# Kernel optimization log

Hardware: AMD Instinct MI355X
Metric: run time of the kernel (lower is better)

The kernel has to match this reference:

```python
import jax, jax.numpy as jnp
import numpy as np

B, S, D, H = 2, 2048, 1024, 16
HD = D // H  # head dim = 64


def setup_inputs() -> dict:
    key = jax.random.key(0)
    ks = jax.random.split(key, 9)
    s_in = 1.0 / np.sqrt(D)
    s_out = 1.0 / np.sqrt(HD)
    return {
        "x": jax.random.normal(ks[0], (B, S, D), jnp.float32),
        "Wq": jax.random.normal(ks[1], (D, H, HD), jnp.float32) * s_in,
        "bq": jnp.zeros((H, HD), jnp.float32),
        "Wk": jax.random.normal(ks[2], (D, H, HD), jnp.float32) * s_in,
        "bk": jnp.zeros((H, HD), jnp.float32),
        "Wv": jax.random.normal(ks[3], (D, H, HD), jnp.float32) * s_in,
        "bv": jnp.zeros((H, HD), jnp.float32),
        "Wo": jax.random.normal(ks[4], (H, HD, D), jnp.float32) * s_out,
        "bo": jnp.zeros((D,), jnp.float32),
    }


def reference(x, Wq, bq, Wk, bk, Wv, bv, Wo, bo):
    # QKV projections: [B,S,D] -> [B,S,H,HD]
    q = jnp.einsum("bsd,dhk->bshk", x, Wq) + bq
    k = jnp.einsum("bsd,dhk->bshk", x, Wk) + bk
    v = jnp.einsum("bsd,dhk->bshk", x, Wv) + bv

    # scaled dot-product attention (matches nnx.dot_product_attention)
    scale = jnp.asarray(1.0 / np.sqrt(HD), q.dtype)
    scores = jnp.einsum("bqhk,bshk->bhqs", q * scale, k)  # [B,H,S,S]
    attn = jax.nn.softmax(scores, axis=-1)
    y = jnp.einsum("bhqs,bshk->bqhk", attn, v)  # [B,S,H,HD]

    # exclusive post-processing: subtract projection onto L2-normalized v
    eps = jnp.asarray(1e-12, v.dtype)
    v_norm = v * jax.lax.rsqrt(jnp.sum(jnp.square(v), axis=-1, keepdims=True) + eps)
    y = y - jnp.sum(y * v_norm, axis=-1, keepdims=True) * v_norm

    # output projection: [B,S,H,HD] -> [B,S,D]
    out = jnp.einsum("bshk,hkd->bsd", y, Wo) + bo
    return out  # dropout is identity (deterministic=True)
```

## Files before the change

kernel.cpp:

```cpp
#include <hip/hip_runtime.h>

#define BB 2
#define SS 2048
#define DD 1024
#define HH 16
#define HDD 64

typedef __attribute__((ext_vector_type(4))) float f32x4;
typedef __attribute__((ext_vector_type(8))) short short8;
typedef __attribute__((ext_vector_type(4))) short short4v;

__device__ __forceinline__ short f2bf(float f) {
    union { float f; unsigned u; } a; a.f = f;
    unsigned r = a.u + 0x7fffu + ((a.u >> 16) & 1u);
    return (short)(r >> 16);
}
__device__ __forceinline__ float bf2f(short s) {
    union { unsigned u; float f; } a; a.u = ((unsigned)(unsigned short)s) << 16;
    return a.f;
}
__device__ __forceinline__ float fast_exp2(float x) {
    float r;
    asm("v_exp_f32 %0, %1\n\ts_nop 0" : "=v"(r) : "v"(x));
    return r;
}
__device__ __forceinline__ unsigned cvt_pk_bf16(float lo, float hi) {
    unsigned r;
    asm("v_cvt_pk_bf16_f32 %0, %1, %2" : "=v"(r) : "v"(lo), "v"(hi));
    return r;
}

#define GLD16(gp, lp) __builtin_amdgcn_global_load_lds( \
    (const __attribute__((address_space(1))) void*)(gp), \
    (__attribute__((address_space(3))) void*)(lp), 16, 0, 0)

__global__ __launch_bounds__(256) void conv_all(
    const float* __restrict__ x,
    const float* __restrict__ Wq, const float* __restrict__ Wk,
    const float* __restrict__ Wv, const float* __restrict__ Wo,
    short* __restrict__ xb, short* __restrict__ Wt, short* __restrict__ Wot,
    float qscale)
{
    const int z = blockIdx.z;
    if (z == 4) {
        const int id = blockIdx.x * 16 + blockIdx.y;
        const size_t base = (size_t)id * 16384 + threadIdx.x * 8;
        #pragma unroll
        for (int it = 0; it < 8; ++it) {
            const size_t i = base + (size_t)it * 2048;
            f32x4 a = *(const f32x4*)(x + i);
            f32x4 b = *(const f32x4*)(x + i + 4);
            short8 o;
            #pragma unroll
            for (int j = 0; j < 4; j++) { o[j] = f2bf(a[j]); o[j + 4] = f2bf(b[j]); }
            *(short8*)(xb + i) = o;
        }
        return;
    }
    __shared__ float t[64][65];
    const float* src = (z == 0) ? Wq : (z == 1) ? Wk : (z == 2) ? Wv : Wo;
    short* dst = (z < 3) ? (Wt + (size_t)z * 1048576) : Wot;
    const float scale = (z == 0) ? qscale : 1.f;

    const int tid = threadIdx.x;
    const int c = tid & 63, rg = tid >> 6;
    const int bi = blockIdx.x * 64, bj = blockIdx.y * 64;
    #pragma unroll
    for (int i = 0; i < 16; i++)
        t[rg * 16 + i][c] = src[(size_t)(bi + rg * 16 + i) * 1024 + bj + c];
    __syncthreads();
    #pragma unroll
    for (int i = 0; i < 16; i++)
        dst[(size_t)(bj + rg * 16 + i) * 1024 + bi + c] = f2bf(scale * t[c][rg * 16 + i]);
}

template<int KIND>
__global__ __launch_bounds__(256, 2) void gemm_mfma(
    const short* __restrict__ A, const short* __restrict__ Bt,
    const float* __restrict__ b0, const float* __restrict__ b1,
    const float* __restrict__ b2, float qscale,
    short* __restrict__ oQ, short* __restrict__ oK, short* __restrict__ oV,
    float* __restrict__ oF)
{
    constexpr int BM = (KIND == 0) ? 128 : 64;
    constexpr int FM = BM / 32;
    constexpr int ASH = BM * 64;
    constexpr int BUFSTR = ASH + 8192;

    __shared__ short lds[2 * BUFSTR];
    const int tid = threadIdx.x;
    const int lane = tid & 63;
    const int ln15 = lane & 15, g = lane >> 4;
    const int swl = ln15 & 7;
    const int wid = tid >> 6;
    const int wm = wid >> 1, wn = wid & 1;
    const int bm = blockIdx.x * BM;
    const int bn = blockIdx.y * 128;
    const bool vpath = (KIND == 0) && (blockIdx.y >= 16);

    f32x4 acc[FM][4];
    #pragma unroll
    for (int i = 0; i < FM; i++)
        #pragma unroll
        for (int j = 0; j < 4; j++) acc[i][j] = (f32x4){0.f, 0.f, 0.f, 0.f};

    const int sr = lane >> 3, cs = lane & 7;
    const int sc8 = (cs ^ sr) << 3;
    const short* Ak = A;
    const short* Bk = Bt;
    int aoff[FM], adst[FM], boff[4], bdst[4];
    #pragma unroll
    for (int j = 0; j < FM; j++) {
        aoff[j] = (bm + wid * (BM / 4) + j * 8 + sr) * 1024 + sc8;
        adst[j] = (wid * (BM / 4) + j * 8) * 64;
    }
    #pragma unroll
    for (int j = 0; j < 4; j++) {
        boff[j] = (bn + wid * 32 + j * 8 + sr) * 1024 + sc8;
        bdst[j] = ASH + (wid * 32 + j * 8) * 64;
    }

    auto stage = [&](int BUF) {
        #pragma unroll
        for (int j = 0; j < FM; j++)
            GLD16(Ak + aoff[j], &lds[BUF * BUFSTR + adst[j]]);
        #pragma unroll
        for (int j = 0; j < 4; j++)
            GLD16(Bk + boff[j], &lds[BUF * BUFSTR + bdst[j]]);
        Ak += 64; Bk += 64;
    };

    const char* ldsc = (const char*)lds;
    int aB[2], bB[2];
    #pragma unroll
    for (int kk = 0; kk < 2; kk++) {
        aB[kk] = (wm * (BM / 2) + ln15) * 128 + ((((kk << 2) | g) ^ swl) << 4);
        bB[kk] = ASH * 2 + (wn * 64 + ln15) * 128 + ((((kk << 2) | g) ^ swl) << 4);
    }

    auto tilec = [&](int BUF) {
        #pragma unroll
        for (int kk = 0; kk < 2; kk++) {
            short8 af[FM], bf[4];
            #pragma unroll
            for (int f = 0; f < FM; f++)
                af[f] = *(const short8*)(ldsc + BUF * (BUFSTR * 2) + aB[kk] + f * 2048);
            #pragma unroll
            for (int f = 0; f < 4; f++)
                bf[f] = *(const short8*)(ldsc + BUF * (BUFSTR * 2) + bB[kk] + f * 2048);
            if (!vpath) {
                #pragma unroll
                for (int fm = 0; fm < FM; fm++)
                    #pragma unroll
                    for (int fn = 0; fn < 4; fn++)
                        acc[fm][fn] = __builtin_amdgcn_mfma_f32_16x16x32_bf16(
                            bf[fn], af[fm], acc[fm][fn], 0, 0, 0);
            } else {
                #pragma unroll
                for (int fm = 0; fm < FM; fm++)
                    #pragma unroll
                    for (int fn = 0; fn < 4; fn++)
                        acc[fm][fn] = __builtin_amdgcn_mfma_f32_16x16x32_bf16(
                            af[fm], bf[fn], acc[fm][fn], 0, 0, 0);
            }
        }
    };

    stage(0);
    asm volatile("s_waitcnt vmcnt(0)" ::: "memory");
    __builtin_amdgcn_s_barrier();

    #pragma unroll 1
    for (int i = 0; i < 7; ++i) {
        stage(1);
        tilec(0);
        asm volatile("s_waitcnt vmcnt(0) lgkmcnt(0)" ::: "memory");
        __builtin_amdgcn_s_barrier();
        stage(0);
        tilec(1);
        asm volatile("s_waitcnt vmcnt(0) lgkmcnt(0)" ::: "memory");
        __builtin_amdgcn_s_barrier();
    }
    stage(1);
    tilec(0);
    asm volatile("s_waitcnt vmcnt(0) lgkmcnt(0)" ::: "memory");
    __builtin_amdgcn_s_barrier();
    tilec(1);

    const int n_base = bn + wn * 64;

    if constexpr (KIND == 1) {
        #pragma unroll
        for (int fn = 0; fn < 4; fn++) {
            const int n0 = n_base + fn * 16 + 4 * g;
            const f32x4 b4 = *(const f32x4*)(b0 + n0);
            #pragma unroll
            for (int fm = 0; fm < FM; fm++) {
                const int t = bm + wm * (BM / 2) + fm * 16 + ln15;
                f32x4 o = acc[fm][fn] + b4;
                *(f32x4*)(oF + (size_t)t * 1024 + n0) = o;
            }
        }
    } else if (!vpath) {
        const bool isq = (n_base < 1024);
        short* dst = isq ? oQ : oK;
        const float* bp = isq ? b0 : b1;
        const float scl = isq ? qscale : 1.f;
        #pragma unroll
        for (int fn = 0; fn < 4; fn++) {
            const int n0 = n_base + fn * 16 + 4 * g;
            const int nl = n0 & 1023;
            f32x4 b4 = *(const f32x4*)(bp + nl);
            b4 *= scl;
            const int h = nl >> 6, d = nl & 63;
            #pragma unroll
            for (int fm = 0; fm < FM; fm++) {
                const int t = bm + wm * (BM / 2) + fm * 16 + ln15;
                const int b = t >> 11, s = t & 2047;
                short4v pk = { f2bf(acc[fm][fn][0] + b4[0]), f2bf(acc[fm][fn][1] + b4[1]),
                               f2bf(acc[fm][fn][2] + b4[2]), f2bf(acc[fm][fn][3] + b4[3]) };
                *(short4v*)(dst + ((size_t)(b * HH + h) * SS + s) * HDD + d) = pk;
            }
        }
    } else {
        #pragma unroll
        for (int fn = 0; fn < 4; fn++) {
            const int nf = n_base + fn * 16 + ln15;
            const int nl = nf - 2048;
            const float bb = b2[nl];
            const int h = nl >> 6, d = nl & 63;
            #pragma unroll
            for (int fm = 0; fm < FM; fm++) {
                const int t0 = bm + wm * (BM / 2) + fm * 16 + 4 * g;
                const int b = t0 >> 11;
                const int sb = (t0 & 2047) & ~63;
                const int pos = g * 16 + (fm & 1) * 4 + ((fm >> 1) & 1) * 8;
                short4v pk = { f2bf(acc[fm][fn][0] + bb), f2bf(acc[fm][fn][1] + bb),
                               f2bf(acc[fm][fn][2] + bb), f2bf(acc[fm][fn][3] + bb) };
                *(short4v*)(oV + ((size_t)(b * HH + h) * HDD + d) * SS + sb + pos) = pk;
            }
        }
    }
}

__global__ __launch_bounds__(256, 2) void attn_mfma_kernel(
    const short* __restrict__ Qh, const short* __restrict__ Kh,
    const short* __restrict__ Vt, short* __restrict__ yb)
{
    __shared__ short lds[32768];

    const int lane = threadIdx.x & 63;
    const int wid  = threadIdx.x >> 6;
    const int ln15 = lane & 15;
    const int g    = lane >> 4;
    const int swl  = ln15 & 7;

    const int bid  = ((int)blockIdx.x & 7) * 64 + ((int)blockIdx.x >> 3);
    const int bh   = bid >> 4;
    const int qB   = (bid & 15) * 128;
    const int qW   = qB + wid * 32;

    const short* qbase = Qh + (size_t)bh * SS * HDD;
    const short* kbase = Kh + (size_t)bh * SS * HDD;
    const short* vtb   = Vt + (size_t)bh * HDD * SS;

    short8 qf[2][2];
    #pragma unroll
    for (int qg = 0; qg < 2; qg++)
        #pragma unroll
        for (int c = 0; c < 2; c++)
            qf[qg][c] = *(const short8*)(qbase +
                (size_t)(qW + qg * 16 + ln15) * HDD + c * 32 + g * 8);

    const short8 ones = { 0x3f80, 0x3f80, 0x3f80, 0x3f80,
                          0x3f80, 0x3f80, 0x3f80, 0x3f80 };

    const int sr = lane >> 3;
    const int cs = lane & 7;
    const int sc8 = (cs ^ sr) << 3;
    const int rvl = lane >> 4;
    const int cc = lane & 15;
    const short* Kk = kbase;
    const short* Vk = vtb;
    int koff[4], kdst[4], voff[4], vdst[4];
    #pragma unroll
    for (int j = 0; j < 4; j++) {
        koff[j] = (wid * 32 + j * 8 + sr) * 64 + sc8;
        kdst[j] = (wid * 32 + j * 8) * 64;
        const int rv = wid * 16 + j * 4 + rvl;
        voff[j] = rv * 2048 + ((cc ^ (rv & 7)) << 3);
        vdst[j] = 8192 + (wid * 16 + j * 4) * 128;
    }

    auto stage = [&](int BUF) {
        #pragma unroll
        for (int j = 0; j < 4; j++)
            GLD16(Kk + koff[j], &lds[BUF * 16384 + kdst[j]]);
        #pragma unroll
        for (int j = 0; j < 4; j++)
            GLD16(Vk + voff[j], &lds[BUF * 16384 + vdst[j]]);
        Kk += 8192; Vk += 128;
    };

    const char* ldsc = (const char*)lds;
    const int kA0 = ln15 * 128 + ((g ^ swl) << 4);
    const int kA1 = ln15 * 128 + (((4 + g) ^ swl) << 4);
    const int vA0 = 16384 + ln15 * 256 + (((2 * g) ^ swl) << 4);
    const int vA1 = 16384 + ln15 * 256 + (((2 * g + 1) ^ swl) << 4);

    f32x4 o[2][4], ol[2];
    #pragma unroll
    for (int qg = 0; qg < 2; qg++) {
        ol[qg] = (f32x4){0.f, 0.f, 0.f, 0.f};
        #pragma unroll
        for (int c = 0; c < 4; c++) o[qg][c] = (f32x4){0.f, 0.f, 0.f, 0.f};
    }

    auto tilec = [&](int BUF) {
        const char* base = ldsc + BUF * 32768;
        f32x4 s[8][2];
        const f32x4 z = {0.f, 0.f, 0.f, 0.f};
        __builtin_amdgcn_s_setprio(1);
        #pragma unroll
        for (int kg = 0; kg < 8; kg++) {
            const short8 k0 = *(const short8*)(base + kA0 + kg * 2048);
            const short8 k1 = *(const short8*)(base + kA1 + kg * 2048);
            #pragma unroll
            for (int qg = 0; qg < 2; qg++) {
                s[kg][qg] = __builtin_amdgcn_mfma_f32_16x16x32_bf16(
                    k0, qf[qg][0], z, 0, 0, 0);
                s[kg][qg] = __builtin_amdgcn_mfma_f32_16x16x32_bf16(
                    k1, qf[qg][1], s[kg][qg], 0, 0, 0);
            }
        }
        __builtin_amdgcn_s_setprio(0);

        union { unsigned u[4]; short8 v; } PA0[2], PA1[2], PB0[2], PB1[2];
        #pragma unroll
        for (int qg = 0; qg < 2; qg++) {
            float p[32];
            #pragma unroll
            for (int kg = 0; kg < 8; kg++)
                #pragma unroll
                for (int r = 0; r < 4; r++)
                    p[kg * 4 + r] = fast_exp2(s[kg][qg][r]);
            PA0[qg].u[0] = cvt_pk_bf16(p[0], p[1]);
            PA0[qg].u[1] = cvt_pk_bf16(p[2], p[3]);
            PA0[qg].u[2] = cvt_pk_bf16(p[4], p[5]);
            PA0[qg].u[3] = cvt_pk_bf16(p[6], p[7]);
            PA1[qg].u[0] = cvt_pk_bf16(p[8], p[9]);
            PA1[qg].u[1] = cvt_pk_bf16(p[10], p[11]);
            PA1[qg].u[2] = cvt_pk_bf16(p[12], p[13]);
            PA1[qg].u[3] = cvt_pk_bf16(p[14], p[15]);
            PB0[qg].u[0] = cvt_pk_bf16(p[16], p[17]);
            PB0[qg].u[1] = cvt_pk_bf16(p[18], p[19]);
            PB0[qg].u[2] = cvt_pk_bf16(p[20], p[21]);
            PB0[qg].u[3] = cvt_pk_bf16(p[22], p[23]);
            PB1[qg].u[0] = cvt_pk_bf16(p[24], p[25]);
            PB1[qg].u[1] = cvt_pk_bf16(p[26], p[27]);
            PB1[qg].u[2] = cvt_pk_bf16(p[28], p[29]);
            PB1[qg].u[3] = cvt_pk_bf16(p[30], p[31]);
        }

        __builtin_amdgcn_s_setprio(1);
        #pragma unroll
        for (int c = 0; c < 4; c++) {
            const short8 vfA0 = *(const short8*)(base + vA0 + c * 4096);
            const short8 vfA1 = *(const short8*)(base + vA1 + c * 4096);
            const short8 vfB0 = *(const short8*)(base + vA0 + c * 4096 + 128);
            const short8 vfB1 = *(const short8*)(base + vA1 + c * 4096 + 128);
            #pragma unroll
            for (int qg = 0; qg < 2; qg++) {
                o[qg][c] = __builtin_amdgcn_mfma_f32_16x16x32_bf16(
                    vfA0, PA0[qg].v, o[qg][c], 0, 0, 0);
                o[qg][c] = __builtin_amdgcn_mfma_f32_16x16x32_bf16(
                    vfA1, PA1[qg].v, o[qg][c], 0, 0, 0);
                o[qg][c] = __builtin_amdgcn_mfma_f32_16x16x32_bf16(
                    vfB0, PB0[qg].v, o[qg][c], 0, 0, 0);
                o[qg][c] = __builtin_amdgcn_mfma_f32_16x16x32_bf16(
                    vfB1, PB1[qg].v, o[qg][c], 0, 0, 0);
            }
        }
        #pragma unroll
        for (int qg = 0; qg < 2; qg++) {
            ol[qg] = __builtin_amdgcn_mfma_f32_16x16x32_bf16(ones, PA0[qg].v, ol[qg], 0, 0, 0);
            ol[qg] = __builtin_amdgcn_mfma_f32_16x16x32_bf16(ones, PA1[qg].v, ol[qg], 0, 0, 0);
            ol[qg] = __builtin_amdgcn_mfma_f32_16x16x32_bf16(ones, PB0[qg].v, ol[qg], 0, 0, 0);
            ol[qg] = __builtin_amdgcn_mfma_f32_16x16x32_bf16(ones, PB1[qg].v, ol[qg], 0, 0, 0);
        }
        __builtin_amdgcn_s_setprio(0);
    };

    stage(0);
    asm volatile("s_waitcnt vmcnt(0)" ::: "memory");
    __builtin_amdgcn_s_barrier();

    #pragma unroll 1
    for (int i = 0; i < 7; ++i) {
        stage(1);
        tilec(0);
        asm volatile("s_waitcnt vmcnt(0) lgkmcnt(0)" ::: "memory");
        __builtin_amdgcn_s_barrier();
        stage(0);
        tilec(1);
        asm volatile("s_waitcnt vmcnt(0) lgkmcnt(0)" ::: "memory");
        __builtin_amdgcn_s_barrier();
    }
    stage(1);
    tilec(0);
    asm volatile("s_waitcnt vmcnt(0) lgkmcnt(0)" ::: "memory");
    __builtin_amdgcn_s_barrier();
    tilec(1);

    const int b = bh >> 4, h = bh & 15;
    #pragma unroll
    for (int qg = 0; qg < 2; qg++) {
        const float inv = 1.f / ol[qg][0];
        #pragma unroll
        for (int c = 0; c < 4; c++) o[qg][c] *= inv;

        const int spos = qB + (wid >> 1) * 64 + (ln15 >> 2) * 16 + qg * 4 +
                         (wid & 1) * 8 + (ln15 & 3);
        float v4[4][4];
        float nv = 0.f, dv = 0.f;
        #pragma unroll
        for (int c = 0; c < 4; c++)
            #pragma unroll
            for (int r = 0; r < 4; r++) {
                const float vd = bf2f(vtb[(size_t)(c * 16 + 4 * g + r) * SS + spos]);
                v4[c][r] = vd;
                nv += vd * vd;
                dv += o[qg][c][r] * vd;
            }
        nv += __shfl_xor(nv, 16); nv += __shfl_xor(nv, 32);
        dv += __shfl_xor(dv, 16); dv += __shfl_xor(dv, 32);
        const float tpp = dv / (nv + 1e-12f);

        const int tok = b * SS + qW + qg * 16 + ln15;
        #pragma unroll
        for (int c = 0; c < 4; c++) {
            short4v pk = { f2bf(o[qg][c][0] - v4[c][0] * tpp),
                           f2bf(o[qg][c][1] - v4[c][1] * tpp),
                           f2bf(o[qg][c][2] - v4[c][2] * tpp),
                           f2bf(o[qg][c][3] - v4[c][3] * tpp) };
            *(short4v*)(yb + (size_t)tok * 1024 + h * 64 + c * 16 + 4 * g) = pk;
        }
    }
}

extern "C" void kernel_launch(void* const* d_in, const int* in_sizes, int n_in,
                              void* d_out, int out_size, void* d_ws, size_t ws_size,
                              hipStream_t stream)
{
    const float* x  = (const float*)d_in[0];
    const float* Wq = (const float*)d_in[1];
    const float* bq = (const float*)d_in[2];
    const float* Wk = (const float*)d_in[3];
    const float* bk = (const float*)d_in[4];
    const float* Wv = (const float*)d_in[5];
    const float* bv = (const float*)d_in[6];
    const float* Wo = (const float*)d_in[7];
    const float* bo = (const float*)d_in[8];
    float* out = (float*)d_out;

    char* w = (char*)d_ws;
    short* xb   = (short*)(w);
    short* Wt   = (short*)(w + (8ull << 20));
    short* Wot  = (short*)(w + (14ull << 20));
    short* Qh   = (short*)(w + (16ull << 20));
    short* Kh   = (short*)(w + (24ull << 20));
    short* Vt   = (short*)(w + (32ull << 20));
    short* yb   = (short*)(w + (40ull << 20));

    const float qscale = 0.125f * 1.44269504f;
    dim3 blk(256);

    conv_all<<<dim3(16, 16, 5), blk, 0, stream>>>(x, Wq, Wk, Wv, Wo,
                                                  xb, Wt, Wot, qscale);

    gemm_mfma<0><<<dim3(32, 24), blk, 0, stream>>>(xb, Wt, bq, bk, bv, qscale,
                                                   Qh, Kh, Vt, nullptr);

    attn_mfma_kernel<<<dim3(512), blk, 0, stream>>>(Qh, Kh, Vt, yb);

    gemm_mfma<1><<<dim3(64, 8), blk, 0, stream>>>(yb, Wot, bo, nullptr, nullptr, 1.f,
                                                  nullptr, nullptr, nullptr, out);
}
```

Measured before the change: 98.72 us.

## Split attention work across 8 waves with 16 query rows each

The attention kernel now launches 512 threads per block, with each of 8 waves handling 16 query rows instead of 4 waves handling 32. K/V staging is spread across the larger wave count, halving per-thread loads. Per-wave registers for accumulators and scores drop. The intent is more parallelism and latency hiding per CU, at the cost of less K/V fragment reuse from LDS per wave and more barrier participants.

```diff
diff --git a/kernel.cpp b/kernel.cpp
--- a/kernel.cpp
+++ b/kernel.cpp
@@ -243,7 +243,7 @@
     }
 }
 
-__global__ __launch_bounds__(256, 2) void attn_mfma_kernel(
+__global__ __launch_bounds__(512) void attn_mfma_kernel(
     const short* __restrict__ Qh, const short* __restrict__ Kh,
     const short* __restrict__ Vt, short* __restrict__ yb)
 {
@@ -258,19 +258,14 @@
     const int bid  = ((int)blockIdx.x & 7) * 64 + ((int)blockIdx.x >> 3);
     const int bh   = bid >> 4;
     const int qB   = (bid & 15) * 128;
-    const int qW   = qB + wid * 32;
+    const int qW   = qB + wid * 16;
 
     const short* qbase = Qh + (size_t)bh * SS * HDD;
     const short* kbase = Kh + (size_t)bh * SS * HDD;
     const short* vtb   = Vt + (size_t)bh * HDD * SS;
 
-    short8 qf[2][2];
-    #pragma unroll
-    for (int qg = 0; qg < 2; qg++)
-        #pragma unroll
-        for (int c = 0; c < 2; c++)
-            qf[qg][c] = *(const short8*)(qbase +
-                (size_t)(qW + qg * 16 + ln15) * HDD + c * 32 + g * 8);
+    const short8 qf0 = *(const short8*)(qbase + (size_t)(qW + ln15) * HDD + g * 8);
+    const short8 qf1 = *(const short8*)(qbase + (size_t)(qW + ln15) * HDD + 32 + g * 8);
 
     const short8 ones = { 0x3f80, 0x3f80, 0x3f80, 0x3f80,
                           0x3f80, 0x3f80, 0x3f80, 0x3f80 };
@@ -282,22 +277,22 @@
     const int cc = lane & 15;
     const short* Kk = kbase;
     const short* Vk = vtb;
-    int koff[4], kdst[4], voff[4], vdst[4];
-    #pragma unroll
-    for (int j = 0; j < 4; j++) {
-        koff[j] = (wid * 32 + j * 8 + sr) * 64 + sc8;
-        kdst[j] = (wid * 32 + j * 8) * 64;
-        const int rv = wid * 16 + j * 4 + rvl;
+    int koff[2], kdst[2], voff[2], vdst[2];
+    #pragma unroll
+    for (int j = 0; j < 2; j++) {
+        koff[j] = (wid * 16 + j * 8 + sr) * 64 + sc8;
+        kdst[j] = (wid * 16 + j * 8) * 64;
+        const int rv = wid * 8 + j * 4 + rvl;
         voff[j] = rv * 2048 + ((cc ^ (rv & 7)) << 3);
-        vdst[j] = 8192 + (wid * 16 + j * 4) * 128;
+        vdst[j] = 8192 + (wid * 8 + j * 4) * 128;
     }
 
     auto stage = [&](int BUF) {
         #pragma unroll
-        for (int j = 0; j < 4; j++)
+        for (int j = 0; j < 2; j++)
             GLD16(Kk + koff[j], &lds[BUF * 16384 + kdst[j]]);
         #pragma unroll
-        for (int j = 0; j < 4; j++)
+        for (int j = 0; j < 2; j++)
             GLD16(Vk + voff[j], &lds[BUF * 16384 + vdst[j]]);
         Kk += 8192; Vk += 128;
     };
@@ -308,59 +303,49 @@
     const int vA0 = 16384 + ln15 * 256 + (((2 * g) ^ swl) << 4);
     const int vA1 = 16384 + ln15 * 256 + (((2 * g + 1) ^ swl) << 4);
 
-    f32x4 o[2][4], ol[2];
-    #pragma unroll
-    for (int qg = 0; qg < 2; qg++) {
-        ol[qg] = (f32x4){0.f, 0.f, 0.f, 0.f};
-        #pragma unroll
-        for (int c = 0; c < 4; c++) o[qg][c] = (f32x4){0.f, 0.f, 0.f, 0.f};
-    }
+    f32x4 o[4], ol;
+    ol = (f32x4){0.f, 0.f, 0.f, 0.f};
+    #pragma unroll
+    for (int c = 0; c < 4; c++) o[c] = (f32x4){0.f, 0.f, 0.f, 0.f};
 
     auto tilec = [&](int BUF) {
         const char* base = ldsc + BUF * 32768;
-        f32x4 s[8][2];
+        f32x4 s[8];
         const f32x4 z = {0.f, 0.f, 0.f, 0.f};
         __builtin_amdgcn_s_setprio(1);
         #pragma unroll
         for (int kg = 0; kg < 8; kg++) {
             const short8 k0 = *(const short8*)(base + kA0 + kg * 2048);
             const short8 k1 = *(const short8*)(base + kA1 + kg * 2048);
-            #pragma unroll
-            for (int qg = 0; qg < 2; qg++) {
-                s[kg][qg] = __builtin_amdgcn_mfma_f32_16x16x32_bf16(
-                    k0, qf[qg][0], z, 0, 0, 0);
-                s[kg][qg] = __builtin_amdgcn_mfma_f32_16x16x32_bf16(
-                    k1, qf[qg][1], s[kg][qg], 0, 0, 0);
-            }
+            s[kg] = __builtin_amdgcn_mfma_f32_16x16x32_bf16(k0, qf0, z, 0, 0, 0);
+            s[kg] = __builtin_amdgcn_mfma_f32_16x16x32_bf16(k1, qf1, s[kg], 0, 0, 0);
         }
         __builtin_amdgcn_s_setprio(0);
 
-        union { unsigned u[4]; short8 v; } PA0[2], PA1[2], PB0[2], PB1[2];
-        #pragma unroll
-        for (int qg = 0; qg < 2; qg++) {
-            float p[32];
-            #pragma unroll
-            for (int kg = 0; kg < 8; kg++)
-                #pragma unroll
-                for (int r = 0; r < 4; r++)
-                    p[kg * 4 + r] = fast_exp2(s[kg][qg][r]);
-            PA0[qg].u[0] = cvt_pk_bf16(p[0], p[1]);
-            PA0[qg].u[1] = cvt_pk_bf16(p[2], p[3]);
-            PA0[qg].u[2] = cvt_pk_bf16(p[4], p[5]);
-            PA0[qg].u[3] = cvt_pk_bf16(p[6], p[7]);
-            PA1[qg].u[0] = cvt_pk_bf16(p[8], p[9]);
-            PA1[qg].u[1] = cvt_pk_bf16(p[10], p[11]);
-            PA1[qg].u[2] = cvt_pk_bf16(p[12], p[13]);
-            PA1[qg].u[3] = cvt_pk_bf16(p[14], p[15]);
-            PB0[qg].u[0] = cvt_pk_bf16(p[16], p[17]);
-            PB0[qg].u[1] = cvt_pk_bf16(p[18], p[19]);
-            PB0[qg].u[2] = cvt_pk_bf16(p[20], p[21]);
-            PB0[qg].u[3] = cvt_pk_bf16(p[22], p[23]);
-            PB1[qg].u[0] = cvt_pk_bf16(p[24], p[25]);
-            PB1[qg].u[1] = cvt_pk_bf16(p[26], p[27]);
-            PB1[qg].u[2] = cvt_pk_bf16(p[28], p[29]);
-            PB1[qg].u[3] = cvt_pk_bf16(p[30], p[31]);
-        }
+        float p[32];
+        #pragma unroll
+        for (int kg = 0; kg < 8; kg++)
+            #pragma unroll
+            for (int r = 0; r < 4; r++)
+                p[kg * 4 + r] = fast_exp2(s[kg][r]);
+
+        union { unsigned u[4]; short8 v; } PA0, PA1, PB0, PB1;
+        PA0.u[0] = cvt_pk_bf16(p[0], p[1]);
+        PA0.u[1] = cvt_pk_bf16(p[2], p[3]);
+        PA0.u[2] = cvt_pk_bf16(p[4], p[5]);
+        PA0.u[3] = cvt_pk_bf16(p[6], p[7]);
+        PA1.u[0] = cvt_pk_bf16(p[8], p[9]);
+        PA1.u[1] = cvt_pk_bf16(p[10], p[11]);
+        PA1.u[2] = cvt_pk_bf16(p[12], p[13]);
+        PA1.u[3] = cvt_pk_bf16(p[14], p[15]);
+        PB0.u[0] = cvt_pk_bf16(p[16], p[17]);
+        PB0.u[1] = cvt_pk_bf16(p[18], p[19]);
+        PB0.u[2] = cvt_pk_bf16(p[20], p[21]);
+        PB0.u[3] = cvt_pk_bf16(p[22], p[23]);
+        PB1.u[0] = cvt_pk_bf16(p[24], p[25]);
+        PB1.u[1] = cvt_pk_bf16(p[26], p[27]);
+        PB1.u[2] = cvt_pk_bf16(p[28], p[29]);
+        PB1.u[3] = cvt_pk_bf16(p[30], p[31]);
 
         __builtin_amdgcn_s_setprio(1);
         #pragma unroll
@@ -369,25 +354,15 @@
             const short8 vfA1 = *(const short8*)(base + vA1 + c * 4096);
             const short8 vfB0 = *(const short8*)(base + vA0 + c * 4096 + 128);
             const short8 vfB1 = *(const short8*)(base + vA1 + c * 4096 + 128);
-            #pragma unroll
-            for (int qg = 0; qg < 2; qg++) {
-                o[qg][c] = __builtin_amdgcn_mfma_f32_16x16x32_bf16(
-                    vfA0, PA0[qg].v, o[qg][c], 0, 0, 0);
-                o[qg][c] = __builtin_amdgcn_mfma_f32_16x16x32_bf16(
-                    vfA1, PA1[qg].v, o[qg][c], 0, 0, 0);
-                o[qg][c] = __builtin_amdgcn_mfma_f32_16x16x32_bf16(
-                    vfB0, PB0[qg].v, o[qg][c], 0, 0, 0);
-                o[qg][c] = __builtin_amdgcn_mfma_f32_16x16x32_bf16(
-                    vfB1, PB1[qg].v, o[qg][c], 0, 0, 0);
-            }
-        }
-        #pragma unroll
-        for (int qg = 0; qg < 2; qg++) {
-            ol[qg] = __builtin_amdgcn_mfma_f32_16x16x32_bf16(ones, PA0[qg].v, ol[qg], 0, 0, 0);
-            ol[qg] = __builtin_amdgcn_mfma_f32_16x16x32_bf16(ones, PA1[qg].v, ol[qg], 0, 0, 0);
-            ol[qg] = __builtin_amdgcn_mfma_f32_16x16x32_bf16(ones, PB0[qg].v, ol[qg], 0, 0, 0);
-            ol[qg] = __builtin_amdgcn_mfma_f32_16x16x32_bf16(ones, PB1[qg].v, ol[qg], 0, 0, 0);
-        }
+            o[c] = __builtin_amdgcn_mfma_f32_16x16x32_bf16(vfA0, PA0.v, o[c], 0, 0, 0);
+            o[c] = __builtin_amdgcn_mfma_f32_16x16x32_bf16(vfA1, PA1.v, o[c], 0, 0, 0);
+            o[c] = __builtin_amdgcn_mfma_f32_16x16x32_bf16(vfB0, PB0.v, o[c], 0, 0, 0);
+            o[c] = __builtin_amdgcn_mfma_f32_16x16x32_bf16(vfB1, PB1.v, o[c], 0, 0, 0);
+        }
+        ol = __builtin_amdgcn_mfma_f32_16x16x32_bf16(ones, PA0.v, ol, 0, 0, 0);
+        ol = __builtin_amdgcn_mfma_f32_16x16x32_bf16(ones, PA1.v, ol, 0, 0, 0);
+        ol = __builtin_amdgcn_mfma_f32_16x16x32_bf16(ones, PB0.v, ol, 0, 0, 0);
+        ol = __builtin_amdgcn_mfma_f32_16x16x32_bf16(ones, PB1.v, ol, 0, 0, 0);
         __builtin_amdgcn_s_setprio(0);
     };
 
@@ -413,38 +388,35 @@
     tilec(1);
 
     const int b = bh >> 4, h = bh & 15;
-    #pragma unroll
-    for (int qg = 0; qg < 2; qg++) {
-        const float inv = 1.f / ol[qg][0];
-        #pragma unroll
-        for (int c = 0; c < 4; c++) o[qg][c] *= inv;
-
-        const int spos = qB + (wid >> 1) * 64 + (ln15 >> 2) * 16 + qg * 4 +
-                         (wid & 1) * 8 + (ln15 & 3);
-        float v4[4][4];
-        float nv = 0.f, dv = 0.f;
-        #pragma unroll
-        for (int c = 0; c < 4; c++)
-            #pragma unroll
-            for (int r = 0; r < 4; r++) {
-                const float vd = bf2f(vtb[(size_t)(c * 16 + 4 * g + r) * SS + spos]);
-                v4[c][r] = vd;
-                nv += vd * vd;
-                dv += o[qg][c][r] * vd;
-            }
-        nv += __shfl_xor(nv, 16); nv += __shfl_xor(nv, 32);
-        dv += __shfl_xor(dv, 16); dv += __shfl_xor(dv, 32);
-        const float tpp = dv / (nv + 1e-12f);
-
-        const int tok = b * SS + qW + qg * 16 + ln15;
-        #pragma unroll
-        for (int c = 0; c < 4; c++) {
-            short4v pk = { f2bf(o[qg][c][0] - v4[c][0] * tpp),
-                           f2bf(o[qg][c][1] - v4[c][1] * tpp),
-                           f2bf(o[qg][c][2] - v4[c][2] * tpp),
-                           f2bf(o[qg][c][3] - v4[c][3] * tpp) };
-            *(short4v*)(yb + (size_t)tok * 1024 + h * 64 + c * 16 + 4 * g) = pk;
-        }
+    const float inv = 1.f / ol[0];
+    #pragma unroll
+    for (int c = 0; c < 4; c++) o[c] *= inv;
+
+    const int spos = qB + (wid >> 2) * 64 + (ln15 >> 2) * 16 + (wid & 1) * 4 +
+                     ((wid >> 1) & 1) * 8 + (ln15 & 3);
+    float v4[4][4];
+    float nv = 0.f, dv = 0.f;
+    #pragma unroll
+    for (int c = 0; c < 4; c++)
+        #pragma unroll
+        for (int r = 0; r < 4; r++) {
+            const float vd = bf2f(vtb[(size_t)(c * 16 + 4 * g + r) * SS + spos]);
+            v4[c][r] = vd;
+            nv += vd * vd;
+            dv += o[c][r] * vd;
+        }
+    nv += __shfl_xor(nv, 16); nv += __shfl_xor(nv, 32);
+    dv += __shfl_xor(dv, 16); dv += __shfl_xor(dv, 32);
+    const float tpp = dv / (nv + 1e-12f);
+
+    const int tok = b * SS + qW + ln15;
+    #pragma unroll
+    for (int c = 0; c < 4; c++) {
+        short4v pk = { f2bf(o[c][0] - v4[c][0] * tpp),
+                       f2bf(o[c][1] - v4[c][1] * tpp),
+                       f2bf(o[c][2] - v4[c][2] * tpp),
+                       f2bf(o[c][3] - v4[c][3] * tpp) };
+        *(short4v*)(yb + (size_t)tok * 1024 + h * 64 + c * 16 + 4 * g) = pk;
     }
 }
 
@@ -481,7 +453,7 @@
     gemm_mfma<0><<<dim3(32, 24), blk, 0, stream>>>(xb, Wt, bq, bk, bv, qscale,
                                                    Qh, Kh, Vt, nullptr);
 
-    attn_mfma_kernel<<<dim3(512), blk, 0, stream>>>(Qh, Kh, Vt, yb);
+    attn_mfma_kernel<<<dim3(512), dim3(512), 0, stream>>>(Qh, Kh, Vt, yb);
 
     gemm_mfma<1><<<dim3(64, 8), blk, 0, stream>>>(yb, Wot, bo, nullptr, nullptr, 1.f,
                                                   nullptr, nullptr, nullptr, out);
```

After: 100.6 us. About the same (+1.9%).

## Split attention tile into QK-exp and PV phases and reschedule the pipeline

Applied to the files above, without the earlier changes.

The per-tile attention body is split into two lambdas: QK^T plus exp into bf16 P fragments, and the PV/rowsum MFMAs. The main loop is reordered so PV for a buffer runs, then a barrier, then the next stage load into that buffer alongside QK-exp on the other buffer. The intent is to shift where global-to-LDS loads overlap with compute and to break the serial dependency inside each tile. In exchange it adds an extra LDS wait and barrier per tile and keeps the P fragments live across barriers, which raises register pressure.

```diff
diff --git a/kernel.cpp b/kernel.cpp
--- a/kernel.cpp
+++ b/kernel.cpp
@@ -292,7 +292,7 @@
         vdst[j] = 8192 + (wid * 16 + j * 4) * 128;
     }
 
-    auto stage = [&](int BUF) {
+    auto stage = [&](const int BUF) {
         #pragma unroll
         for (int j = 0; j < 4; j++)
             GLD16(Kk + koff[j], &lds[BUF * 16384 + kdst[j]]);
@@ -316,7 +316,10 @@
         for (int c = 0; c < 4; c++) o[qg][c] = (f32x4){0.f, 0.f, 0.f, 0.f};
     }
 
-    auto tilec = [&](int BUF) {
+    union Pk { unsigned u[4]; short8 v; };
+    Pk PA0[2], PA1[2], PB0[2], PB1[2];
+
+    auto qkexp = [&](const int BUF) {
         const char* base = ldsc + BUF * 32768;
         f32x4 s[8][2];
         const f32x4 z = {0.f, 0.f, 0.f, 0.f};
@@ -335,7 +338,6 @@
         }
         __builtin_amdgcn_s_setprio(0);
 
-        union { unsigned u[4]; short8 v; } PA0[2], PA1[2], PB0[2], PB1[2];
         #pragma unroll
         for (int qg = 0; qg < 2; qg++) {
             float p[32];
@@ -361,7 +363,10 @@
             PB1[qg].u[2] = cvt_pk_bf16(p[28], p[29]);
             PB1[qg].u[3] = cvt_pk_bf16(p[30], p[31]);
         }
-
+    };
+
+    auto pv = [&](const int BUF) {
+        const char* base = ldsc + BUF * 32768;
         __builtin_amdgcn_s_setprio(1);
         #pragma unroll
         for (int c = 0; c < 4; c++) {
@@ -391,26 +396,26 @@
         __builtin_amdgcn_s_setprio(0);
     };
 
+#define LGKM0 asm volatile("s_waitcnt lgkmcnt(0)" ::: "memory")
+#define WAITV0 asm volatile("s_waitcnt vmcnt(0) lgkmcnt(0)" ::: "memory")
+#define BARR __builtin_amdgcn_s_barrier()
+
     stage(0);
-    asm volatile("s_waitcnt vmcnt(0)" ::: "memory");
-    __builtin_amdgcn_s_barrier();
+    WAITV0; BARR;
+    stage(1); qkexp(0); WAITV0; BARR;
 
     #pragma unroll 1
     for (int i = 0; i < 7; ++i) {
-        stage(1);
-        tilec(0);
-        asm volatile("s_waitcnt vmcnt(0) lgkmcnt(0)" ::: "memory");
-        __builtin_amdgcn_s_barrier();
-        stage(0);
-        tilec(1);
-        asm volatile("s_waitcnt vmcnt(0) lgkmcnt(0)" ::: "memory");
-        __builtin_amdgcn_s_barrier();
-    }
-    stage(1);
-    tilec(0);
-    asm volatile("s_waitcnt vmcnt(0) lgkmcnt(0)" ::: "memory");
-    __builtin_amdgcn_s_barrier();
-    tilec(1);
+        pv(0); LGKM0; BARR; stage(0); qkexp(1); WAITV0; BARR;
+        pv(1); LGKM0; BARR; stage(1); qkexp(0); WAITV0; BARR;
+    }
+    pv(0);
+    qkexp(1);
+    pv(1);
+
+#undef LGKM0
+#undef WAITV0
+#undef BARR
 
     const int b = bh >> 4, h = bh & 15;
     #pragma unroll
```

Result: no change. 100.2 us (+1.5%).
